# Optimization experiments

Measured on AMD Instinct MI355X. Metric: run time of the kernel, lower is better.

## Reference

```python
import jax, jax.numpy as jnp
import numpy as np


def _make_pert(r, s):
    lin = np.linspace(-r, r, s)
    xm, ym, tm = np.meshgrid(lin, lin, lin)  # default 'xy' indexing, matches torch code
    return jnp.asarray(np.stack([xm.ravel(), ym.ravel(), tm.ravel()], axis=-1), dtype=jnp.float32)

PERTS = (_make_pert(0.01, 3), _make_pert(0.05, 5), _make_pert(0.09, 7))  # [27,3],[125,3],[343,3]

N, IN, H, HQ, FF, OUT = 4096, 3, 256, 64, 64, 3


def setup_inputs():
    key = jax.random.key(0)
    ks = jax.random.split(key, 24)

    def W(k, i, o):
        return (jax.random.normal(k, (i, o), jnp.float32) / np.sqrt(i)).astype(jnp.float32)

    one = jnp.ones((1,), jnp.float32)
    return {
        "x": jax.random.normal(ks[0], (N, 1), jnp.float32),
        "y": jax.random.normal(ks[1], (N, 1), jnp.float32),
        "t": jax.random.normal(ks[2], (N, 1), jnp.float32),
        # linear_emb: 3 -> 64 -> WaveAct -> 256
        "emb_W1": W(ks[3], IN, HQ), "emb_b1": jnp.zeros((HQ,), jnp.float32),
        "emb_wa": one, "emb_wb": one,
        "emb_W2": W(ks[4], HQ, H), "emb_b2": jnp.zeros((H,), jnp.float32),
        # multiregion_mixer: 4 -> 8 -> WaveAct -> 1
        "mix_W1": W(ks[5], 4, 8), "mix_b1": jnp.zeros((8,), jnp.float32),
        "mix_wa": one, "mix_wb": one,
        "mix_W2": W(ks[6], 8, 1), "mix_b2": jnp.zeros((1,), jnp.float32),
        "out_W0": W(ks[7], H, FF), "out_b0": jnp.zeros((FF,), jnp.float32),
        "out_wa0": one, "out_wb0": one,
        "out_Wh": jnp.stack([W(ks[8 + i], FF, FF) for i in range(3)]),
        "out_bh": jnp.zeros((3, FF), jnp.float32),
        "out_wah": jnp.ones((3, 1), jnp.float32), "out_wbh": jnp.ones((3, 1), jnp.float32),
        "out_Wf1": W(ks[11], FF, FF), "out_bf1": jnp.zeros((FF,), jnp.float32),
        "out_waf": one, "out_wbf": one,
        "out_Wf2": W(ks[12], FF, OUT), "out_bf2": jnp.zeros((OUT,), jnp.float32),
    }


def _wave(h, wa, wb):
    return wa * jnp.sin(h) + wb * jnp.cos(h)


def reference(x, y, t,
              emb_W1, emb_b1, emb_wa, emb_wb, emb_W2, emb_b2,
              mix_W1, mix_b1, mix_wa, mix_wb, mix_W2, mix_b2,
              out_W0, out_b0, out_wa0, out_wb0,
              out_Wh, out_bh, out_wah, out_wbh,
              out_Wf1, out_bf1, out_waf, out_wbf, out_Wf2, out_bf2):
    def emb(s):  # [..., 3] -> [..., 256]
        h = _wave(s @ emb_W1 + emb_b1, emb_wa, emb_wb)
        return h @ emb_W2 + emb_b2

    src = jnp.concatenate([x, y, t], axis=-1)           # [N, 3]
    feats = [emb(src)]                                   # region 1: unperturbed
    for P in PERTS:
        perturbed = src[:, None, :] + P[None, :, :]      # [N, P, 3]
        feats.append(emb(perturbed).mean(axis=1))        # [N, 256]
    stacked = jnp.stack(feats, axis=-1)                  # [N, 256, 4] (== permute(0,2,1) of stack dim=1)

    m = _wave(stacked @ mix_W1 + mix_b1, mix_wa, mix_wb) # [N, 256, 8]
    e = (m @ mix_W2 + mix_b2)[:, :, 0]                   # [N, 256]

    h = _wave(e @ out_W0 + out_b0, out_wa0, out_wb0)     # [N, 64]
    for i in range(3):                                   # fixed num_layer-1 = 3 hidden layers
        h = _wave(h @ out_Wh[i] + out_bh[i], out_wah[i], out_wbh[i])
    h = _wave(h @ out_Wf1 + out_bf1, out_waf, out_wbf)
    return h @ out_Wf2 + out_bf2                         # [N, 3]
```

## Files before the change

kernel.cpp:

```cpp
#include <hip/hip_runtime.h>

#define SPB 2

__device__ __forceinline__ float rl(float v, int l) {
    return __builtin_bit_cast(float, __builtin_amdgcn_readlane(__builtin_bit_cast(int, v), l));
}
__device__ __forceinline__ float blo(unsigned d) { return __builtin_bit_cast(float, d << 16); }
__device__ __forceinline__ float bhi(unsigned d) { return __builtin_bit_cast(float, d & 0xffff0000u); }
__device__ __forceinline__ unsigned pack_bf16(float a, float b) {
    unsigned ua = __builtin_bit_cast(unsigned, a);
    unsigned ub = __builtin_bit_cast(unsigned, b);
    ua = (ua + 0x7fffu + ((ua >> 16) & 1u)) >> 16;
    ub = (ub + 0x7fffu + ((ub >> 16) & 1u)) >> 16;
    return ua | (ub << 16);
}

#define WS_C    0
#define WS_W0P  256
#define WS_WHP  (256 + 8192)
#define WS_WF1P (256 + 8192 + 6144)

__global__ __launch_bounds__(256) void preprocess(
    const float* __restrict__ embW1,
    const float* __restrict__ outW0, const float* __restrict__ outWh,
    const float* __restrict__ outWf1, unsigned* __restrict__ ws)
{
    const int g = blockIdx.x * 256 + threadIdx.x;
    if (g < 8192) {
        const int k2 = g >> 6, f = g & 63;
        ws[WS_W0P + g] = pack_bf16(outW0[(2*k2)*64 + f], outW0[(2*k2+1)*64 + f]);
    } else if (g < 14336) {
        const int i = g - 8192;
        const int layer = i >> 11, r = i & 2047;
        const int k2 = r >> 6, f = r & 63;
        const float* W = outWh + layer*4096;
        ws[WS_WHP + i] = pack_bf16(W[(2*k2)*64 + f], W[(2*k2+1)*64 + f]);
    } else if (g < 16384) {
        const int i = g - 14336;
        const int k2 = i >> 6, f = i & 63;
        ws[WS_WF1P + i] = pack_bf16(outWf1[(2*k2)*64 + f], outWf1[(2*k2+1)*64 + f]);
    } else if (g < 16576) {
        const int i = g - 16384;
        const int r = i >> 6, ch = i & 63;
        const float w0 = embW1[ch], w1 = embW1[64 + ch], w2 = embW1[128 + ch];
        float v;
        if (r == 0) {
            v = (1.f + 2.f*__cosf(0.01f*w0)) * (1.f + 2.f*__cosf(0.01f*w1))
              * (1.f + 2.f*__cosf(0.01f*w2)) * (1.f/27.f);
        } else if (r == 1) {
            v = (1.f + 2.f*(__cosf(0.025f*w0) + __cosf(0.05f*w0)))
              * (1.f + 2.f*(__cosf(0.025f*w1) + __cosf(0.05f*w1)))
              * (1.f + 2.f*(__cosf(0.025f*w2) + __cosf(0.05f*w2))) * (1.f/125.f);
        } else {
            v = (1.f + 2.f*(__cosf(0.03f*w0) + __cosf(0.06f*w0) + __cosf(0.09f*w0)))
              * (1.f + 2.f*(__cosf(0.03f*w1) + __cosf(0.06f*w1) + __cosf(0.09f*w1)))
              * (1.f + 2.f*(__cosf(0.03f*w2) + __cosf(0.06f*w2) + __cosf(0.09f*w2))) * (1.f/343.f);
        }
        ((float*)ws)[WS_C + i] = v;
    }
}

__global__ __launch_bounds__(256, 8) void model_fused(
    const float* __restrict__ x, const float* __restrict__ y, const float* __restrict__ t,
    const float* __restrict__ embW1, const float* __restrict__ embb1,
    const float* __restrict__ embwa, const float* __restrict__ embwb,
    const float* __restrict__ embW2, const float* __restrict__ embb2,
    const float* __restrict__ mixW1, const float* __restrict__ mixb1,
    const float* __restrict__ mixwa, const float* __restrict__ mixwb,
    const float* __restrict__ mixW2, const float* __restrict__ mixb2,
    const float* __restrict__ outb0,
    const float* __restrict__ outwa0, const float* __restrict__ outwb0,
    const float* __restrict__ outbh,
    const float* __restrict__ outwah, const float* __restrict__ outwbh,
    const float* __restrict__ outbf1,
    const float* __restrict__ outwaf, const float* __restrict__ outwbf,
    const float* __restrict__ outWf2, const float* __restrict__ outbf2,
    const unsigned* __restrict__ ws,
    float* __restrict__ out, int N)
{
    __shared__ float se[SPB][256];
    __shared__ float pf[2][SPB][64];
    __shared__ float sh[2][SPB][64];

    const int tid  = threadIdx.x;
    const int lane = tid & 63;
    const int n0   = blockIdx.x * SPB;

    float swv0, swv1, cv1, cv2, cv3;
    {
        const float w0 = embW1[lane], w1 = embW1[64 + lane], w2 = embW1[128 + lane];
        const float bb = embb1[lane];
        const float ewa = embwa[0], ewb = embwb[0];
        const int ns0 = n0;
        const int ns1 = (n0 + 1 < N) ? n0 + 1 : N - 1;
        const float u0 = fmaf(x[ns0], w0, fmaf(y[ns0], w1, fmaf(t[ns0], w2, bb)));
        const float u1 = fmaf(x[ns1], w0, fmaf(y[ns1], w1, fmaf(t[ns1], w2, bb)));
        swv0 = ewa*__sinf(u0) + ewb*__cosf(u0);
        swv1 = ewa*__sinf(u1) + ewb*__cosf(u1);
        const float* C = (const float*)ws + WS_C;
        cv1 = C[lane]; cv2 = C[64 + lane]; cv3 = C[128 + lane];
    }

    {
        const int c = tid;
        float a00=0.f,a01=0.f,a02=0.f,a03=0.f;
        float a10=0.f,a11=0.f,a12=0.f,a13=0.f;

        #pragma unroll 16
        for (int ch = 0; ch < 64; ++ch) {
            const float w  = embW2[ch*256 + c];
            const float s0 = rl(swv0, ch), s1 = rl(swv1, ch);
            const float k1 = rl(cv1, ch), k2 = rl(cv2, ch), k3 = rl(cv3, ch);
            const float t0 = s0 * w, t1 = s1 * w;
            a00 += t0; a01 = fmaf(t0,k1,a01); a02 = fmaf(t0,k2,a02); a03 = fmaf(t0,k3,a03);
            a10 += t1; a11 = fmaf(t1,k1,a11); a12 = fmaf(t1,k2,a12); a13 = fmaf(t1,k3,a13);
        }

        const float mwa = mixwa[0], mwb = mixwb[0], mb2 = mixb2[0];
        const float bb2 = embb2[c];
        {
            const float s0 = a00+bb2, s1 = a01+bb2, s2 = a02+bb2, s3 = a03+bb2;
            float ev = mb2;
            #pragma unroll
            for (int j = 0; j < 8; ++j) {
                float p = fmaf(s0, mixW1[j],
                          fmaf(s1, mixW1[8 + j],
                          fmaf(s2, mixW1[16 + j],
                          fmaf(s3, mixW1[24 + j], mixb1[j]))));
                ev = fmaf(mwa*__sinf(p) + mwb*__cosf(p), mixW2[j], ev);
            }
            se[0][c] = ev;
        }
        {
            const float s0 = a10+bb2, s1 = a11+bb2, s2 = a12+bb2, s3 = a13+bb2;
            float ev = mb2;
            #pragma unroll
            for (int j = 0; j < 8; ++j) {
                float p = fmaf(s0, mixW1[j],
                          fmaf(s1, mixW1[8 + j],
                          fmaf(s2, mixW1[16 + j],
                          fmaf(s3, mixW1[24 + j], mixb1[j]))));
                ev = fmaf(mwa*__sinf(p) + mwb*__cosf(p), mixW2[j], ev);
            }
            se[1][c] = ev;
        }
    }
    __syncthreads();

    const int h = tid >> 7, n = (tid >> 6) & 1, f = tid & 63;

    {
        const unsigned* W0p = ws + WS_W0P;
        float p = 0.f;
        #pragma unroll 8
        for (int j = h*32; j < h*32 + 32; ++j) {
            const float4 a4 = *(const float4*)&se[n][4*j];
            const unsigned d0 = W0p[(2*j)*64 + f];
            const unsigned d1 = W0p[(2*j+1)*64 + f];
            p = fmaf(a4.x, blo(d0), p); p = fmaf(a4.y, bhi(d0), p);
            p = fmaf(a4.z, blo(d1), p); p = fmaf(a4.w, bhi(d1), p);
        }
        pf[h][n][f] = p;
    }
    __syncthreads();
    if (tid < 128) {
        const float a = pf[0][n][f] + pf[1][n][f] + outb0[f];
        sh[0][n][f] = outwa0[0]*__sinf(a) + outwb0[0]*__cosf(a);
    }
    __syncthreads();

    int cur = 0;
    #pragma unroll
    for (int i = 0; i < 4; ++i) {
        const unsigned* Wp = (i < 3) ? (ws + WS_WHP + i*2048) : (ws + WS_WF1P);
        float p = 0.f;
        #pragma unroll
        for (int j = 0; j < 8; ++j) {
            const int jj = h*8 + j;
            const float4 a4 = *(const float4*)&sh[cur][n][4*jj];
            const unsigned d0 = Wp[(2*jj)*64 + f];
            const unsigned d1 = Wp[(2*jj+1)*64 + f];
            p = fmaf(a4.x, blo(d0), p); p = fmaf(a4.y, bhi(d0), p);
            p = fmaf(a4.z, blo(d1), p); p = fmaf(a4.w, bhi(d1), p);
        }
        pf[h][n][f] = p;
        __syncthreads();
        if (tid < 128) {
            float a = pf[0][n][f] + pf[1][n][f];
            float wa, wb;
            if (i < 3) { a += outbh[i*64 + f]; wa = outwah[i]; wb = outwbh[i]; }
            else       { a += outbf1[f];       wa = outwaf[0]; wb = outwbf[0]; }
            sh[1 - cur][n][f] = wa*__sinf(a) + wb*__cosf(a);
        }
        __syncthreads();
        cur ^= 1;
    }

    if (tid < SPB*3) {
        const int nn = tid / 3, o = tid - nn*3;
        float a = outbf2[o];
        #pragma unroll 8
        for (int k = 0; k < 64; ++k)
            a = fmaf(sh[cur][nn][k], outWf2[k*3 + o], a);
        const int gn = n0 + nn;
        if (gn < N) out[gn*3 + o] = a;
    }
}

extern "C" void kernel_launch(void* const* d_in, const int* in_sizes, int n_in,
                              void* d_out, int out_size, void* d_ws, size_t ws_size,
                              hipStream_t stream) {
    const float* x      = (const float*)d_in[0];
    const float* y      = (const float*)d_in[1];
    const float* t      = (const float*)d_in[2];
    const float* embW1  = (const float*)d_in[3];
    const float* embb1  = (const float*)d_in[4];
    const float* embwa  = (const float*)d_in[5];
    const float* embwb  = (const float*)d_in[6];
    const float* embW2  = (const float*)d_in[7];
    const float* embb2  = (const float*)d_in[8];
    const float* mixW1  = (const float*)d_in[9];
    const float* mixb1  = (const float*)d_in[10];
    const float* mixwa  = (const float*)d_in[11];
    const float* mixwb  = (const float*)d_in[12];
    const float* mixW2  = (const float*)d_in[13];
    const float* mixb2  = (const float*)d_in[14];
    const float* outW0  = (const float*)d_in[15];
    const float* outb0  = (const float*)d_in[16];
    const float* outwa0 = (const float*)d_in[17];
    const float* outwb0 = (const float*)d_in[18];
    const float* outWh  = (const float*)d_in[19];
    const float* outbh  = (const float*)d_in[20];
    const float* outwah = (const float*)d_in[21];
    const float* outwbh = (const float*)d_in[22];
    const float* outWf1 = (const float*)d_in[23];
    const float* outbf1 = (const float*)d_in[24];
    const float* outwaf = (const float*)d_in[25];
    const float* outwbf = (const float*)d_in[26];
    const float* outWf2 = (const float*)d_in[27];
    const float* outbf2 = (const float*)d_in[28];
    float* out = (float*)d_out;
    unsigned* ws = (unsigned*)d_ws;

    const int N = in_sizes[0];

    preprocess<<<65, 256, 0, stream>>>(embW1, outW0, outWh, outWf1, ws);

    const int blocks = (N + SPB - 1) / SPB;
    model_fused<<<blocks, 256, 0, stream>>>(
        x, y, t,
        embW1, embb1, embwa, embwb, embW2, embb2,
        mixW1, mixb1, mixwa, mixwb, mixW2, mixb2,
        outb0, outwa0, outwb0,
        outbh, outwah, outwbh,
        outbf1, outwaf, outwbf, outWf2, outbf2,
        ws, out, N);
}
```

Measured before the change: 150.1 us.

## Process four samples per block with one wave per sample in MLP tail

Each block now handles four samples instead of two, so every embW2 weight load is reused across four samples, and the region coefficients are read as uniform loads instead of readlanes. The tail MLP maps one wavefront per sample and broadcasts activations with readlane. This removes the shared-memory partial sums and most of the __syncthreads barriers between layers. In exchange there are more registers per thread, a lower occupancy hint (launch bounds 4), and half as many blocks. The final output layer reads hfin written by other lanes of the same wave without a barrier, so it relies on wave-synchronous execution.

```diff
diff --git a/kernel.cpp b/kernel.cpp
--- a/kernel.cpp
+++ b/kernel.cpp
@@ -1,6 +1,6 @@
 #include <hip/hip_runtime.h>
 
-#define SPB 2
+#define SPB 4
 
 __device__ __forceinline__ float rl(float v, int l) {
     return __builtin_bit_cast(float, __builtin_amdgcn_readlane(__builtin_bit_cast(int, v), l));
@@ -60,7 +60,7 @@
     }
 }
 
-__global__ __launch_bounds__(256, 8) void model_fused(
+__global__ __launch_bounds__(256, 4) void model_fused(
     const float* __restrict__ x, const float* __restrict__ y, const float* __restrict__ t,
     const float* __restrict__ embW1, const float* __restrict__ embb1,
     const float* __restrict__ embwa, const float* __restrict__ embwb,
@@ -79,131 +79,117 @@
     float* __restrict__ out, int N)
 {
     __shared__ float se[SPB][256];
-    __shared__ float pf[2][SPB][64];
-    __shared__ float sh[2][SPB][64];
+    __shared__ float hfin[SPB][64];
 
     const int tid  = threadIdx.x;
     const int lane = tid & 63;
+    const int wv   = tid >> 6;
     const int n0   = blockIdx.x * SPB;
 
-    float swv0, swv1, cv1, cv2, cv3;
+    float swv0, swv1, swv2, swv3;
     {
         const float w0 = embW1[lane], w1 = embW1[64 + lane], w2 = embW1[128 + lane];
         const float bb = embb1[lane];
         const float ewa = embwa[0], ewb = embwb[0];
         const int ns0 = n0;
         const int ns1 = (n0 + 1 < N) ? n0 + 1 : N - 1;
+        const int ns2 = (n0 + 2 < N) ? n0 + 2 : N - 1;
+        const int ns3 = (n0 + 3 < N) ? n0 + 3 : N - 1;
         const float u0 = fmaf(x[ns0], w0, fmaf(y[ns0], w1, fmaf(t[ns0], w2, bb)));
         const float u1 = fmaf(x[ns1], w0, fmaf(y[ns1], w1, fmaf(t[ns1], w2, bb)));
+        const float u2 = fmaf(x[ns2], w0, fmaf(y[ns2], w1, fmaf(t[ns2], w2, bb)));
+        const float u3 = fmaf(x[ns3], w0, fmaf(y[ns3], w1, fmaf(t[ns3], w2, bb)));
         swv0 = ewa*__sinf(u0) + ewb*__cosf(u0);
         swv1 = ewa*__sinf(u1) + ewb*__cosf(u1);
-        const float* C = (const float*)ws + WS_C;
-        cv1 = C[lane]; cv2 = C[64 + lane]; cv3 = C[128 + lane];
+        swv2 = ewa*__sinf(u2) + ewb*__cosf(u2);
+        swv3 = ewa*__sinf(u3) + ewb*__cosf(u3);
     }
 
     {
         const int c = tid;
-        float a00=0.f,a01=0.f,a02=0.f,a03=0.f;
-        float a10=0.f,a11=0.f,a12=0.f,a13=0.f;
+        const float* Cw = (const float*)ws;
+        float acc[4][4];
+        #pragma unroll
+        for (int s = 0; s < 4; ++s)
+            #pragma unroll
+            for (int r = 0; r < 4; ++r) acc[s][r] = 0.f;
 
         #pragma unroll 16
         for (int ch = 0; ch < 64; ++ch) {
             const float w  = embW2[ch*256 + c];
+            const float k1 = Cw[ch], k2 = Cw[64 + ch], k3 = Cw[128 + ch];
             const float s0 = rl(swv0, ch), s1 = rl(swv1, ch);
-            const float k1 = rl(cv1, ch), k2 = rl(cv2, ch), k3 = rl(cv3, ch);
-            const float t0 = s0 * w, t1 = s1 * w;
-            a00 += t0; a01 = fmaf(t0,k1,a01); a02 = fmaf(t0,k2,a02); a03 = fmaf(t0,k3,a03);
-            a10 += t1; a11 = fmaf(t1,k1,a11); a12 = fmaf(t1,k2,a12); a13 = fmaf(t1,k3,a13);
+            const float s2 = rl(swv2, ch), s3 = rl(swv3, ch);
+            const float t0 = s0*w, t1 = s1*w, t2 = s2*w, t3 = s3*w;
+            acc[0][0] += t0; acc[0][1] = fmaf(t0,k1,acc[0][1]); acc[0][2] = fmaf(t0,k2,acc[0][2]); acc[0][3] = fmaf(t0,k3,acc[0][3]);
+            acc[1][0] += t1; acc[1][1] = fmaf(t1,k1,acc[1][1]); acc[1][2] = fmaf(t1,k2,acc[1][2]); acc[1][3] = fmaf(t1,k3,acc[1][3]);
+            acc[2][0] += t2; acc[2][1] = fmaf(t2,k1,acc[2][1]); acc[2][2] = fmaf(t2,k2,acc[2][2]); acc[2][3] = fmaf(t2,k3,acc[2][3]);
+            acc[3][0] += t3; acc[3][1] = fmaf(t3,k1,acc[3][1]); acc[3][2] = fmaf(t3,k2,acc[3][2]); acc[3][3] = fmaf(t3,k3,acc[3][3]);
         }
 
         const float mwa = mixwa[0], mwb = mixwb[0], mb2 = mixb2[0];
         const float bb2 = embb2[c];
-        {
-            const float s0 = a00+bb2, s1 = a01+bb2, s2 = a02+bb2, s3 = a03+bb2;
+        #pragma unroll
+        for (int s = 0; s < 4; ++s) {
+            const float f0 = acc[s][0]+bb2, f1 = acc[s][1]+bb2;
+            const float f2 = acc[s][2]+bb2, f3 = acc[s][3]+bb2;
             float ev = mb2;
             #pragma unroll
             for (int j = 0; j < 8; ++j) {
-                float p = fmaf(s0, mixW1[j],
-                          fmaf(s1, mixW1[8 + j],
-                          fmaf(s2, mixW1[16 + j],
-                          fmaf(s3, mixW1[24 + j], mixb1[j]))));
+                float p = fmaf(f0, mixW1[j],
+                          fmaf(f1, mixW1[8 + j],
+                          fmaf(f2, mixW1[16 + j],
+                          fmaf(f3, mixW1[24 + j], mixb1[j]))));
                 ev = fmaf(mwa*__sinf(p) + mwb*__cosf(p), mixW2[j], ev);
             }
-            se[0][c] = ev;
-        }
-        {
-            const float s0 = a10+bb2, s1 = a11+bb2, s2 = a12+bb2, s3 = a13+bb2;
-            float ev = mb2;
-            #pragma unroll
-            for (int j = 0; j < 8; ++j) {
-                float p = fmaf(s0, mixW1[j],
-                          fmaf(s1, mixW1[8 + j],
-                          fmaf(s2, mixW1[16 + j],
-                          fmaf(s3, mixW1[24 + j], mixb1[j]))));
-                ev = fmaf(mwa*__sinf(p) + mwb*__cosf(p), mixW2[j], ev);
-            }
-            se[1][c] = ev;
+            se[s][c] = ev;
         }
     }
     __syncthreads();
 
-    const int h = tid >> 7, n = (tid >> 6) & 1, f = tid & 63;
-
+    const int f = lane, n = wv;
+    float h;
     {
         const unsigned* W0p = ws + WS_W0P;
-        float p = 0.f;
-        #pragma unroll 8
-        for (int j = h*32; j < h*32 + 32; ++j) {
+        float p0 = 0.f, p1 = 0.f, p2 = 0.f, p3 = 0.f;
+        #pragma unroll 16
+        for (int j = 0; j < 64; ++j) {
             const float4 a4 = *(const float4*)&se[n][4*j];
             const unsigned d0 = W0p[(2*j)*64 + f];
             const unsigned d1 = W0p[(2*j+1)*64 + f];
-            p = fmaf(a4.x, blo(d0), p); p = fmaf(a4.y, bhi(d0), p);
-            p = fmaf(a4.z, blo(d1), p); p = fmaf(a4.w, bhi(d1), p);
-        }
-        pf[h][n][f] = p;
-    }
-    __syncthreads();
-    if (tid < 128) {
-        const float a = pf[0][n][f] + pf[1][n][f] + outb0[f];
-        sh[0][n][f] = outwa0[0]*__sinf(a) + outwb0[0]*__cosf(a);
-    }
-    __syncthreads();
-
-    int cur = 0;
+            p0 = fmaf(a4.x, blo(d0), p0); p1 = fmaf(a4.y, bhi(d0), p1);
+            p2 = fmaf(a4.z, blo(d1), p2); p3 = fmaf(a4.w, bhi(d1), p3);
+        }
+        const float a = (p0 + p1) + (p2 + p3) + outb0[f];
+        h = outwa0[0]*__sinf(a) + outwb0[0]*__cosf(a);
+    }
+
     #pragma unroll
     for (int i = 0; i < 4; ++i) {
         const unsigned* Wp = (i < 3) ? (ws + WS_WHP + i*2048) : (ws + WS_WF1P);
-        float p = 0.f;
+        float p0 = 0.f, p1 = 0.f;
         #pragma unroll
-        for (int j = 0; j < 8; ++j) {
-            const int jj = h*8 + j;
-            const float4 a4 = *(const float4*)&sh[cur][n][4*jj];
-            const unsigned d0 = Wp[(2*jj)*64 + f];
-            const unsigned d1 = Wp[(2*jj+1)*64 + f];
-            p = fmaf(a4.x, blo(d0), p); p = fmaf(a4.y, bhi(d0), p);
-            p = fmaf(a4.z, blo(d1), p); p = fmaf(a4.w, bhi(d1), p);
-        }
-        pf[h][n][f] = p;
-        __syncthreads();
-        if (tid < 128) {
-            float a = pf[0][n][f] + pf[1][n][f];
-            float wa, wb;
-            if (i < 3) { a += outbh[i*64 + f]; wa = outwah[i]; wb = outwbh[i]; }
-            else       { a += outbf1[f];       wa = outwaf[0]; wb = outwbf[0]; }
-            sh[1 - cur][n][f] = wa*__sinf(a) + wb*__cosf(a);
-        }
-        __syncthreads();
-        cur ^= 1;
-    }
-
-    if (tid < SPB*3) {
-        const int nn = tid / 3, o = tid - nn*3;
-        float a = outbf2[o];
-        #pragma unroll 8
+        for (int j = 0; j < 32; ++j) {
+            const unsigned d = Wp[j*64 + f];
+            const float hk0 = rl(h, 2*j), hk1 = rl(h, 2*j + 1);
+            p0 = fmaf(hk0, blo(d), p0);
+            p1 = fmaf(hk1, bhi(d), p1);
+        }
+        float a = p0 + p1;
+        float wa, wb;
+        if (i < 3) { a += outbh[i*64 + f]; wa = outwah[i]; wb = outwbh[i]; }
+        else       { a += outbf1[f];       wa = outwaf[0]; wb = outwbf[0]; }
+        h = wa*__sinf(a) + wb*__cosf(a);
+    }
+
+    hfin[n][f] = h;
+    if (f < 3) {
+        float a = outbf2[f];
+        #pragma unroll 16
         for (int k = 0; k < 64; ++k)
-            a = fmaf(sh[cur][nn][k], outWf2[k*3 + o], a);
-        const int gn = n0 + nn;
-        if (gn < N) out[gn*3 + o] = a;
+            a = fmaf(hfin[n][k], outWf2[k*3 + f], a);
+        const int gn = n0 + n;
+        if (gn < N) out[gn*3 + f] = a;
     }
 }
 
```

After: 143.3 us. -4.5%, faster.
